# Optimization experiments

Hardware: AMD Instinct MI355X
Metric: run time of the kernel (lower is better)

Reference implementation:

```python
import jax, jax.numpy as jnp
import numpy as np

B, C, H, W = 16, 256, 64, 64
K = 3


def _binary_act(x):
    # forward: sign(x); backward: piecewise-polynomial STE surrogate out3
    sg = jax.lax.stop_gradient
    f32 = x.dtype
    m1 = (x < -1).astype(f32)
    m2 = (x < 0).astype(f32)
    m3 = (x < 1).astype(f32)
    out1 = -1.0 * m1 + (x * x + 2.0 * x) * (1.0 - m1)
    out2 = out1 * m2 + (-x * x + 2.0 * x) * (1.0 - m2)
    out3 = out2 * m3 + 1.0 * (1.0 - m3)
    return sg(jnp.sign(x)) - sg(out3) + out3


def _binarize_weight(w):
    # per-output-channel scale * sign(w) in forward; clipped identity STE in backward
    sg = jax.lax.stop_gradient
    scale = sg(jnp.mean(jnp.abs(w), axis=(1, 2, 3), keepdims=True))  # (O,1,1,1)
    bw_no_grad = scale * jnp.sign(w)
    cw = jnp.clip(w, -1.0, 1.0)
    return sg(bw_no_grad) - sg(cw) + cw


def setup_inputs() -> dict:
    key = jax.random.key(0)
    k1, k2 = jax.random.split(key, 2)
    x = jax.random.normal(k1, (B, C, H, W), dtype=jnp.float32)
    conv_w = jax.random.normal(k2, (C, C, K, K), dtype=jnp.float32) * 0.05
    move0_bias = jnp.zeros((1, C, 1, 1), dtype=jnp.float32)
    pr_bias0 = jnp.zeros((1, C, 1, 1), dtype=jnp.float32)
    prelu_alpha = jnp.full((C,), 0.25, dtype=jnp.float32)  # torch PReLU default
    pr_bias1 = jnp.zeros((1, C, 1, 1), dtype=jnp.float32)
    return {"x": x, "move0_bias": move0_bias, "conv_w": conv_w,
            "pr_bias0": pr_bias0, "prelu_alpha": prelu_alpha, "pr_bias1": pr_bias1}


def reference(x, move0_bias, conv_w, pr_bias0, prelu_alpha, pr_bias1):
    out = x + move0_bias                       # LearnableBias move0
    out = _binary_act(out)                     # BinaryActivation (values in {-1,0,1})
    bw = _binarize_weight(conv_w)              # HardBinaryConv weight binarization
    pad = K // 2
    out = jax.lax.conv_general_dilated(
        out, bw, window_strides=(1, 1), padding=((pad, pad), (pad, pad)),
        dimension_numbers=("NCHW", "OIHW", "NCHW"))
    # RPReLU: bias0 -> per-channel PReLU -> bias1
    out = out + pr_bias0
    a = prelu_alpha.reshape(1, -1, 1, 1)
    out = jnp.where(out >= 0, out, a * out)
    out = out + pr_bias1
    return out + x                             # residual
```

## Files before the change

kernel.cpp:

```cpp
#include <hip/hip_runtime.h>
#include <hip/hip_bf16.h>
#include <stdint.h>

#define B_ 16
#define C_ 256
#define H_ 64
#define W_ 64
#define WP 66
#define HP 66
#define ROWB (WP * 128)
#define STAGEB (3 * ROWB + 32)

typedef __attribute__((ext_vector_type(4))) float f32x4;
typedef __attribute__((ext_vector_type(4))) int int4v;
typedef __attribute__((ext_vector_type(8))) int int8v;

typedef const __attribute__((address_space(1))) uint32_t* gptr_t;
typedef __attribute__((address_space(3))) uint32_t* lptr_t;

__device__ __forceinline__ void gl_lds16(const void* g, void* l) {
  __builtin_amdgcn_global_load_lds((gptr_t)g, (lptr_t)l, 16, 0, 0);
}

__device__ __forceinline__ uint8_t sgn4(float v) {
  return v > 0.f ? (uint8_t)0x2 : (v < 0.f ? (uint8_t)0xA : (uint8_t)0);
}

#define EXT8(v4) __builtin_shufflevector((v4), (v4), 0, 1, 2, 3, -1, -1, -1, -1)

__global__ void prep_and_binarize(const float* __restrict__ w,
                                  float* __restrict__ scale,
                                  uint8_t* __restrict__ wtb,
                                  const float* __restrict__ x,
                                  const float* __restrict__ bias,
                                  uint8_t* __restrict__ a_p) {
  int tid = threadIdx.x;
  if (blockIdx.x < 256) {
    int o = blockIdx.x, c = tid;
    const float* wo = w + (size_t)o * 2304 + (size_t)c * 9;
    float v[9];
    float s = 0.f;
#pragma unroll
    for (int t = 0; t < 9; ++t) { v[t] = wo[t]; s += fabsf(v[t]); }
    __shared__ float red[256];
    __shared__ uint8_t sg[9][256];
    red[c] = s;
#pragma unroll
    for (int t = 0; t < 9; ++t) sg[t][c] = sgn4(v[t]);
    __syncthreads();
    for (int st = 128; st > 0; st >>= 1) {
      if (c < st) red[c] += red[c + st];
      __syncthreads();
    }
    if (c == 0) scale[o] = red[0] / 2304.0f;
    if (c < 128) {
      int k = c;
      int ot = o >> 6, mi = (o >> 4) & 3, lm = o & 15;
      int kh = k >> 6, lk = (k >> 4) & 3, jb = k & 15;
      int l = lk * 16 + lm;
#pragma unroll
      for (int t = 0; t < 9; ++t) {
        uint8_t byte = (uint8_t)(sg[t][2 * k] | (sg[t][2 * k + 1] << 4));
        wtb[((((size_t)t * 4 + ot) * 2 + kh) * 4 + mi) * 1024 + l * 16 + jb] = byte;
      }
    }
    return;
  }
  int id = blockIdx.x - 256;
  int bh = id >> 2, b = bh >> 6, h = bh & 63, c0 = (id & 3) * 64;
  __shared__ uint8_t lt[64][72];
#pragma unroll
  for (int p = 0; p < 4; ++p) {
    int ci = p * 16 + (tid >> 4), w4 = (tid & 15) * 4;
    f32x4 v = *(const f32x4*)(x + (((size_t)(b * C_ + c0 + ci) * H_ + h) * W_ + w4));
    float bb = bias[c0 + ci];
#pragma unroll
    for (int k = 0; k < 4; ++k) lt[w4 + k][ci] = sgn4(v[k] + bb);
  }
  __syncthreads();
  size_t rowbase = (size_t)(b * HP + h + 1) * ROWB;
#pragma unroll
  for (int r = 0; r < 2; ++r) {
    int u = r * 256 + tid;
    int w_ = u >> 3, q = u & 7;
    uint32_t val = 0;
#pragma unroll
    for (int e = 0; e < 8; ++e)
      val |= (uint32_t)(lt[w_][q * 8 + e] & 15) << (4 * e);
    int wp = w_ + 1;
    int ch = (c0 + q * 8) >> 5;
    int pos = wp * 128 + (((ch ^ wp) & 7) << 4) + (q & 3) * 4;
    *(uint32_t*)(a_p + rowbase + pos) = val;
  }
  if ((id & 3) == 0) {
    if (tid < 32) *(uint32_t*)(a_p + rowbase + tid * 4) = 0;
    else if (tid < 64) *(uint32_t*)(a_p + rowbase + 65 * 128 + (tid - 32) * 4) = 0;
  }
  if (h == 0) {
    uint32_t* zr = (uint32_t*)(a_p + (size_t)b * HP * ROWB) + (id & 3) * 528;
    for (int k = tid; k < 528; k += 256) zr[k] = 0;
  } else if (h == 63) {
    uint32_t* zr = (uint32_t*)(a_p + ((size_t)b * HP + 65) * ROWB) + (id & 3) * 528;
    for (int k = tid; k < 528; k += 256) zr[k] = 0;
  }
}

#define LOADW(dst, t, kh) {                                                       \
  const uint8_t* wb_ = wtb + ((((size_t)(t) * 4 + wv) * 2 + (kh)) * 4) * 1024 + l * 16; \
  _Pragma("unroll") for (int mi = 0; mi < 4; ++mi)                                \
      dst[mi] = *(const int4v*)(wb_ + mi * 1024); }

#define LOADB(dst, d, dxi, kh) {                                                  \
  int ch_ = (kh) * 4 + lk;                                                        \
  _Pragma("unroll") for (int ni = 0; ni < 4; ++ni) {                              \
    int wp_ = ni * 16 + lm + (dxi);                                               \
    dst[ni] = *(const int4v*)(smem + (d) * ROWB + wp_ * 128 +                     \
                              (((ch_ ^ wp_) & 7) << 4)); } }

#define MFMA_BURST(wreg)                                                          \
  __builtin_amdgcn_s_setprio(1);                                                  \
  _Pragma("unroll") for (int mi = 0; mi < 4; ++mi)                                \
    _Pragma("unroll") for (int ni = 0; ni < 4; ++ni)                              \
      acc[mi][ni] = __builtin_amdgcn_mfma_scale_f32_16x16x128_f8f6f4(             \
          EXT8(wreg[mi]), EXT8(bf[ni]), acc[mi][ni], 4, 4, 0, 127, 0, 127);       \
  __builtin_amdgcn_s_setprio(0);

__global__ __launch_bounds__(256, 3) void bconv(
    const uint8_t* __restrict__ a_p, const uint8_t* __restrict__ wtb,
    const float* __restrict__ scale, const float* __restrict__ x,
    const float* __restrict__ pb0, const float* __restrict__ alpha,
    const float* __restrict__ pb1, float* __restrict__ out) {
  __shared__ __attribute__((aligned(16))) uint8_t smem[STAGEB];
  int bh = (blockIdx.x & 7) * 128 + (blockIdx.x >> 3);
  int b = bh >> 6, h = bh & 63;
  int tid = threadIdx.x, l = tid & 63, wv = tid >> 6;
  int lm = l & 15, lk = l >> 4;
  int wm = wv * 64;

  const uint8_t* src = a_p + (size_t)(b * HP + h) * ROWB;
#pragma unroll
  for (int it = 0; it < 6; ++it)
    gl_lds16(src + (size_t)(it * 256 + tid) * 16, smem + it * 4096 + wv * 1024);
  if (tid < 48) gl_lds16(src + 24576 + (size_t)tid * 16, smem + 24576);

  f32x4 acc[4][4];
#pragma unroll
  for (int i = 0; i < 4; ++i)
#pragma unroll
    for (int j = 0; j < 4; ++j) acc[i][j] = (f32x4){0.f, 0.f, 0.f, 0.f};

  asm volatile("s_waitcnt vmcnt(0)" ::: "memory");
  __syncthreads();

  int4v wA[4], wB[4], bf[4];
  LOADW(wA, 0, 0)
#pragma unroll 1
  for (int t = 0; t < 9; ++t) {
    int d = t / 3, dxi = t - d * 3;
    LOADW(wB, t, 1)
    LOADB(bf, d, dxi, 0)
    MFMA_BURST(wA)
    if (t < 8) { LOADW(wA, t + 1, 0) }
    LOADB(bf, d, dxi, 1)
    MFMA_BURST(wB)
  }

  size_t xb = (size_t)b * C_ * H_ * W_ + (size_t)h * W_;
#pragma unroll
  for (int mi = 0; mi < 4; ++mi) {
#pragma unroll
    for (int j = 0; j < 4; ++j) {
      int o = wm + mi * 16 + lk * 4 + j;
      float sc = scale[o], b0 = pb0[o], al = alpha[o], b1 = pb1[o];
      size_t rowo = xb + (size_t)o * (H_ * W_);
#pragma unroll
      for (int ni = 0; ni < 4; ++ni) {
        int wcol = ni * 16 + lm;
        float v = acc[mi][ni][j] * sc + b0;
        v = v >= 0.f ? v : al * v;
        v = v + b1 + x[rowo + wcol];
        out[rowo + wcol] = v;
      }
    }
  }
}

extern "C" void kernel_launch(void* const* d_in, const int* in_sizes, int n_in,
                              void* d_out, int out_size, void* d_ws, size_t ws_size,
                              hipStream_t stream) {
  const float* x     = (const float*)d_in[0];
  const float* m0b   = (const float*)d_in[1];
  const float* w     = (const float*)d_in[2];
  const float* pb0   = (const float*)d_in[3];
  const float* alpha = (const float*)d_in[4];
  const float* pb1   = (const float*)d_in[5];
  float* out = (float*)d_out;

  float* scale = (float*)d_ws;
  uint8_t* wtb = (uint8_t*)d_ws + 4096;
  uint8_t* a_p = (uint8_t*)d_ws + 4096 + (size_t)9 * 4 * 2 * 4 * 1024 + 1024;

  hipLaunchKernelGGL(prep_and_binarize, dim3(256 + B_ * H_ * 4), dim3(256), 0,
                     stream, w, scale, wtb, x, m0b, a_p);
  hipLaunchKernelGGL(bconv, dim3(B_ * H_), dim3(256), 0, stream,
                     a_p, wtb, scale, x, pb0, alpha, pb1, out);
}
```

Baseline: 50.42 us.

## Switch binary conv MFMA from 16x16x128 to 32x32x64 FP4 tiles

```diff
diff --git a/kernel.cpp b/kernel.cpp
--- a/kernel.cpp
+++ b/kernel.cpp
@@ -12,6 +12,7 @@
 #define STAGEB (3 * ROWB + 32)
 
 typedef __attribute__((ext_vector_type(4))) float f32x4;
+typedef __attribute__((ext_vector_type(16))) float f32x16;
 typedef __attribute__((ext_vector_type(4))) int int4v;
 typedef __attribute__((ext_vector_type(8))) int int8v;
 
@@ -55,13 +56,13 @@
     if (c == 0) scale[o] = red[0] / 2304.0f;
     if (c < 128) {
       int k = c;
-      int ot = o >> 6, mi = (o >> 4) & 3, lm = o & 15;
-      int kh = k >> 6, lk = (k >> 4) & 3, jb = k & 15;
-      int l = lk * 16 + lm;
+      int ot = o >> 6, mi = (o >> 5) & 1, lrow = o & 31;
+      int kq = k >> 5, khalf = (k >> 4) & 1, jb = k & 15;
+      int l = khalf * 32 + lrow;
 #pragma unroll
       for (int t = 0; t < 9; ++t) {
         uint8_t byte = (uint8_t)(sg[t][2 * k] | (sg[t][2 * k + 1] << 4));
-        wtb[((((size_t)t * 4 + ot) * 2 + kh) * 4 + mi) * 1024 + l * 16 + jb] = byte;
+        wtb[(((((size_t)t * 4 + ot) * 4 + kq) * 2 + mi) * 64 + l) * 16 + jb] = byte;
       }
     }
     return;
@@ -106,23 +107,27 @@
 }
 
 #define LOADW(dst, t, kh) {                                                       \
-  const uint8_t* wb_ = wtb + ((((size_t)(t) * 4 + wv) * 2 + (kh)) * 4) * 1024 + l * 16; \
-  _Pragma("unroll") for (int mi = 0; mi < 4; ++mi)                                \
-      dst[mi] = *(const int4v*)(wb_ + mi * 1024); }
+  _Pragma("unroll") for (int q = 0; q < 2; ++q)                                   \
+  _Pragma("unroll") for (int mi = 0; mi < 2; ++mi)                                \
+      dst[q * 2 + mi] = *(const int4v*)(wtb +                                     \
+        (((((size_t)(t) * 4 + wv) * 4 + (kh) * 2 + q) * 2 + mi) * 64 + l) * 16); }
 
 #define LOADB(dst, d, dxi, kh) {                                                  \
-  int ch_ = (kh) * 4 + lk;                                                        \
-  _Pragma("unroll") for (int ni = 0; ni < 4; ++ni) {                              \
-    int wp_ = ni * 16 + lm + (dxi);                                               \
-    dst[ni] = *(const int4v*)(smem + (d) * ROWB + wp_ * 128 +                     \
-                              (((ch_ ^ wp_) & 7) << 4)); } }
-
-#define MFMA_BURST(wreg)                                                          \
+  _Pragma("unroll") for (int q = 0; q < 2; ++q)                                   \
+  _Pragma("unroll") for (int ni = 0; ni < 2; ++ni) {                              \
+    int wp_ = ni * 32 + (l & 31) + (dxi);                                         \
+    int ch_ = ((kh) * 2 + q) * 2 + (l >> 5);                                      \
+    dst[q * 2 + ni] = *(const int4v*)(smem + (d) * ROWB + wp_ * 128 +             \
+                                      (((ch_ ^ wp_) & 7) << 4)); } }
+
+#define MFMA_BURST(wreg, breg)                                                    \
   __builtin_amdgcn_s_setprio(1);                                                  \
-  _Pragma("unroll") for (int mi = 0; mi < 4; ++mi)                                \
-    _Pragma("unroll") for (int ni = 0; ni < 4; ++ni)                              \
-      acc[mi][ni] = __builtin_amdgcn_mfma_scale_f32_16x16x128_f8f6f4(             \
-          EXT8(wreg[mi]), EXT8(bf[ni]), acc[mi][ni], 4, 4, 0, 127, 0, 127);       \
+  _Pragma("unroll") for (int q = 0; q < 2; ++q)       \
+  _Pragma("unroll") for (int mi = 0; mi < 2; ++mi)   \
+  _Pragma("unroll") for (int ni = 0; ni < 2; ++ni)                                \
+      acc[mi][ni] = __builtin_amdgcn_mfma_scale_f32_32x32x64_f8f6f4(              \
+          EXT8(wreg[q * 2 + mi]), EXT8(breg[q * 2 + ni]), acc[mi][ni],            \
+          4, 4, 0, 127, 0, 127);                                                  \
   __builtin_amdgcn_s_setprio(0);
 
 __global__ __launch_bounds__(256, 3) void bconv(
@@ -134,7 +139,6 @@
   int bh = (blockIdx.x & 7) * 128 + (blockIdx.x >> 3);
   int b = bh >> 6, h = bh & 63;
   int tid = threadIdx.x, l = tid & 63, wv = tid >> 6;
-  int lm = l & 15, lk = l >> 4;
   int wm = wv * 64;
 
   const uint8_t* src = a_p + (size_t)(b * HP + h) * ROWB;
@@ -143,11 +147,11 @@
     gl_lds16(src + (size_t)(it * 256 + tid) * 16, smem + it * 4096 + wv * 1024);
   if (tid < 48) gl_lds16(src + 24576 + (size_t)tid * 16, smem + 24576);
 
-  f32x4 acc[4][4];
-#pragma unroll
-  for (int i = 0; i < 4; ++i)
-#pragma unroll
-    for (int j = 0; j < 4; ++j) acc[i][j] = (f32x4){0.f, 0.f, 0.f, 0.f};
+  f32x16 acc[2][2];
+#pragma unroll
+  for (int i = 0; i < 2; ++i)
+#pragma unroll
+    for (int j = 0; j < 2; ++j) acc[i][j] = (f32x16)(0.f);
 
   asm volatile("s_waitcnt vmcnt(0)" ::: "memory");
   __syncthreads();
@@ -159,24 +163,25 @@
     int d = t / 3, dxi = t - d * 3;
     LOADW(wB, t, 1)
     LOADB(bf, d, dxi, 0)
-    MFMA_BURST(wA)
+    MFMA_BURST(wA, bf)
     if (t < 8) { LOADW(wA, t + 1, 0) }
     LOADB(bf, d, dxi, 1)
-    MFMA_BURST(wB)
+    MFMA_BURST(wB, bf)
   }
 
   size_t xb = (size_t)b * C_ * H_ * W_ + (size_t)h * W_;
-#pragma unroll
-  for (int mi = 0; mi < 4; ++mi) {
-#pragma unroll
-    for (int j = 0; j < 4; ++j) {
-      int o = wm + mi * 16 + lk * 4 + j;
+  int lhi = l >> 5;
+#pragma unroll
+  for (int mi = 0; mi < 2; ++mi) {
+#pragma unroll
+    for (int r = 0; r < 16; ++r) {
+      int o = wm + mi * 32 + (r & 3) + 8 * (r >> 2) + 4 * lhi;
       float sc = scale[o], b0 = pb0[o], al = alpha[o], b1 = pb1[o];
       size_t rowo = xb + (size_t)o * (H_ * W_);
 #pragma unroll
-      for (int ni = 0; ni < 4; ++ni) {
-        int wcol = ni * 16 + lm;
-        float v = acc[mi][ni][j] * sc + b0;
+      for (int ni = 0; ni < 2; ++ni) {
+        int wcol = ni * 32 + (l & 31);
+        float v = acc[mi][ni][r] * sc + b0;
         v = v >= 0.f ? v : al * v;
         v = v + b1 + x[rowo + wcol];
         out[rowo + wcol] = v;
@@ -198,7 +203,7 @@
 
   float* scale = (float*)d_ws;
   uint8_t* wtb = (uint8_t*)d_ws + 4096;
-  uint8_t* a_p = (uint8_t*)d_ws + 4096 + (size_t)9 * 4 * 2 * 4 * 1024 + 1024;
+  uint8_t* a_p = (uint8_t*)d_ws + 4096 + (size_t)9 * 4 * 4 * 2 * 1024 + 1024;
 
   hipLaunchKernelGGL(prep_and_binarize, dim3(256 + B_ * H_ * 4), dim3(256), 0,
                      stream, w, scale, wtb, x, m0b, a_p);
```

Result: no change. 51.14 us (+1.4%).
